# Performance work log

Measured on AMD Instinct MI355X. Metric: run time of the kernel, lower is better.

## Reference

```python
import jax, jax.numpy as jnp
import numpy as np

EPS = 1e-5
NEG = -1e20


def layer_norm(x, gamma, beta):
    mu = jnp.mean(x, axis=-1, keepdims=True)
    var = jnp.mean(jnp.square(x - mu), axis=-1, keepdims=True)
    return (x - mu) * jax.lax.rsqrt(var + EPS) * gamma + beta


def setup_inputs() -> dict:
    key = jax.random.key(0)
    ks = jax.random.split(key, 12)
    B, S, D, H, HD = 2, 2048, 1024, 16, 64
    hid = H * HD
    inp = {
        "q": jax.random.normal(ks[0], (B, S, D), jnp.float32),
        "k": jax.random.normal(ks[1], (B, S, D), jnp.float32),
        "v": jax.random.normal(ks[2], (B, S, D), jnp.float32),
        "mask": jax.random.randint(ks[3], (B, 1, S, S), 0, 2, jnp.int32),
        "Wq": jax.random.normal(ks[4], (D, hid), jnp.float32) * (D ** -0.5),
        "bq": jnp.zeros((hid,), jnp.float32),
        "Wk": jax.random.normal(ks[5], (D, hid), jnp.float32) * (D ** -0.5),
        "bk": jnp.zeros((hid,), jnp.float32),
        "Wv": jax.random.normal(ks[6], (D, hid), jnp.float32) * (D ** -0.5),
        "bv": jnp.zeros((hid,), jnp.float32),
        "Wo": jax.random.normal(ks[7], (hid, D), jnp.float32) * (hid ** -0.5),
        "bo": jnp.zeros((D,), jnp.float32),
        "gamma": jnp.ones((D,), jnp.float32),
        "beta": jnp.zeros((D,), jnp.float32),
    }
    return inp


def reference(q, k, v, mask, Wq, bq, Wk, bk, Wv, bv, Wo, bo, gamma, beta):
    B, S, D = q.shape
    H, HD = 16, 64
    scale = HD ** -0.5
    qh = (layer_norm(q, gamma, beta) @ Wq + bq).reshape(B, S, H, HD).transpose(0, 2, 1, 3)
    kh = (layer_norm(k, gamma, beta) @ Wk + bk).reshape(B, S, H, HD).transpose(0, 2, 1, 3)
    vh = (layer_norm(v, gamma, beta) @ Wv + bv).reshape(B, S, H, HD).transpose(0, 2, 1, 3)
    dots = jnp.einsum('bhqd,bhkd->bhqk', qh, kh)  # [B,H,S,S]
    dots = jnp.where(mask == 0, NEG, dots) * scale  # mask BEFORE scale (as in source)
    attn = jax.nn.softmax(dots, axis=-1)
    out = jnp.einsum('bhqk,bhkd->bhqd', attn, vh)  # [B,H,S,HD]
    # Faithful to `out.view(B, S, -1)` on a [B,H,S,HD]-contiguous tensor: raw reshape,
    # no head transpose.
    out = out.reshape(B, S, H * HD)
    return out @ Wo + bo
```

## Files before the change

### kernel.cpp

```cpp
#include <hip/hip_runtime.h>

typedef short short8 __attribute__((ext_vector_type(8)));
typedef float f32x4 __attribute__((ext_vector_type(4)));

#define QSCALE 0.18033688011112042f

__device__ __forceinline__ unsigned short f2bf(float f) {
  unsigned u = __builtin_bit_cast(unsigned, f);
  u += 0x7fffu + ((u >> 16) & 1u);
  return (unsigned short)(u >> 16);
}

__device__ __forceinline__ void gload16(const void* g, void* l) {
  typedef __attribute__((address_space(1))) unsigned int gas;
  typedef __attribute__((address_space(3))) unsigned int las;
  __builtin_amdgcn_global_load_lds((gas*)(unsigned long long)g,
                                   (las*)(unsigned)(unsigned long long)l, 16, 0, 0);
}

#define MFMA16(a, b, c) __builtin_amdgcn_mfma_f32_16x16x32_bf16(a, b, c, 0, 0, 0)

__global__ __launch_bounds__(256) void wtrans_kernel(
    const float* __restrict__ Wq, const float* __restrict__ Wk,
    const float* __restrict__ Wv, const float* __restrict__ Wo,
    unsigned short* __restrict__ Wt) {
  const int wsel = blockIdx.z;
  const float* W = wsel == 0 ? Wq : wsel == 1 ? Wk : wsel == 2 ? Wv : Wo;
  const float wscale = (wsel == 0) ? QSCALE : 1.0f;
  unsigned short* out = Wt + (long)wsel * 1048576;
  __shared__ float lds[64][65];
  const int t = threadIdx.x;
  const int k0 = blockIdx.x * 64, n0 = blockIdx.y * 64;
#pragma unroll
  for (int i = 0; i < 4; ++i) {
    int r = (t >> 4) + i * 16, c4 = (t & 15) * 4;
    float4 vv = *(const float4*)(W + (long)(k0 + r) * 1024 + n0 + c4);
    lds[r][c4] = vv.x; lds[r][c4 + 1] = vv.y; lds[r][c4 + 2] = vv.z; lds[r][c4 + 3] = vv.w;
  }
  __syncthreads();
#pragma unroll
  for (int i = 0; i < 16; ++i) {
    int flat = t + i * 256;
    int n = flat >> 6, kk = flat & 63;
    out[(long)(n0 + n) * 1024 + k0 + kk] = f2bf(lds[kk][n] * wscale);
  }
}

__global__ __launch_bounds__(256) void maskpack_kernel(const int* __restrict__ mask,
                                                       unsigned* __restrict__ bits) {
  const long n = 8388608;
  const long stride = (long)gridDim.x * 256;
  const int lane = threadIdx.x & 63;
  for (long i = (long)blockIdx.x * 256 + threadIdx.x; i < n; i += stride) {
    unsigned long long bal = __ballot(mask[i] != 0);
    if ((lane & 31) == 0) bits[i >> 5] = (unsigned)(bal >> (lane & 32));
  }
}

__global__ __launch_bounds__(256) void ln_kernel(
    const float* __restrict__ q, const float* __restrict__ k, const float* __restrict__ v,
    const float* __restrict__ gamma, const float* __restrict__ beta,
    unsigned short* __restrict__ lnq, unsigned short* __restrict__ lnk,
    unsigned short* __restrict__ lnv) {
  const int row = blockIdx.x, which = blockIdx.y;
  const float* x = (which == 0 ? q : which == 1 ? k : v) + (long)row * 1024;
  unsigned short* y = (which == 0 ? lnq : which == 1 ? lnk : lnv) + (long)row * 1024;
  const int t = threadIdx.x, lane = t & 63, wv = t >> 6;
  float4 xv = ((const float4*)x)[t];
  float s = xv.x + xv.y + xv.z + xv.w;
  float s2 = xv.x * xv.x + xv.y * xv.y + xv.z * xv.z + xv.w * xv.w;
#pragma unroll
  for (int off = 32; off > 0; off >>= 1) {
    s += __shfl_down(s, off);
    s2 += __shfl_down(s2, off);
  }
  __shared__ float red[8];
  if (lane == 0) { red[wv] = s; red[wv + 4] = s2; }
  __syncthreads();
  float tot = red[0] + red[1] + red[2] + red[3];
  float tot2 = red[4] + red[5] + red[6] + red[7];
  float mu = tot * (1.0f / 1024.0f);
  float var = tot2 * (1.0f / 1024.0f) - mu * mu;
  float rs = rsqrtf(var + 1e-5f);
  float4 g = ((const float4*)gamma)[t];
  float4 be = ((const float4*)beta)[t];
  ushort4 o;
  o.x = f2bf((xv.x - mu) * rs * g.x + be.x);
  o.y = f2bf((xv.y - mu) * rs * g.y + be.y);
  o.z = f2bf((xv.z - mu) * rs * g.z + be.z);
  o.w = f2bf((xv.w - mu) * rs * g.w + be.w);
  ((ushort4*)y)[t] = o;
}

template <int BM, int MODE>
__global__ __launch_bounds__(256) void gemm_kernel(
    const unsigned short* __restrict__ A0, const unsigned short* __restrict__ A1,
    const unsigned short* __restrict__ A2, const unsigned short* __restrict__ Wt,
    const float* __restrict__ b0, const float* __restrict__ b1,
    const float* __restrict__ b2, unsigned short* __restrict__ outB,
    unsigned short* __restrict__ outV, float* __restrict__ outF) {
  constexpr int BK = 64;
  constexpr int MI = BM / 32;
  const int z = blockIdx.z;
  const unsigned short* A = z == 0 ? A0 : z == 1 ? A1 : A2;
  const unsigned short* Bt = Wt + (long)z * 1048576;
  const float* bias = z == 0 ? b0 : z == 1 ? b1 : b2;
  unsigned short* outz = outB + (long)z * 4194304;
  const float bscale = (MODE == 0 && z == 0) ? QSCALE : 1.0f;

  __shared__ char lds[BM * 128 + 16384];
  char* As = lds;
  char* Bs = lds + BM * 128;
  const int tid = threadIdx.x, lane = tid & 63, w = tid >> 6;
  const int wr = w >> 1, wc = w & 1;
  const int m0 = blockIdx.x * BM, n0 = blockIdx.y * 128;
  constexpr int K = 1024;
  constexpr int ACH = BM * 8 / 256;

  f32x4 acc[MI][4] = {};
  for (int kt = 0; kt < K / BK; ++kt) {
    __syncthreads();
#pragma unroll
    for (int i = 0; i < ACH; ++i) {
      int c = tid + i * 256;
      int row = c >> 3, pg = (c & 7) ^ (row & 7);
      gload16(A + (long)(m0 + row) * K + kt * BK + pg * 8, As + c * 16);
    }
#pragma unroll
    for (int i = 0; i < 4; ++i) {
      int c = tid + i * 256;
      int row = c >> 3, pg = (c & 7) ^ (row & 7);
      gload16(Bt + (long)(n0 + row) * K + kt * BK + pg * 8, Bs + c * 16);
    }
    asm volatile("s_waitcnt vmcnt(0)" ::: "memory");
    __syncthreads();
#pragma unroll
    for (int ks = 0; ks < 2; ++ks) {
      short8 af[MI], bf[4];
#pragma unroll
      for (int mi = 0; mi < MI; ++mi) {
        int row = wr * (BM / 2) + mi * 16 + (lane & 15);
        int part = (ks * 4 + (lane >> 4)) ^ (row & 7);
        af[mi] = *(const short8*)(As + row * 128 + part * 16);
      }
#pragma unroll
      for (int ni = 0; ni < 4; ++ni) {
        int row = wc * 64 + ni * 16 + (lane & 15);
        int part = (ks * 4 + (lane >> 4)) ^ (row & 7);
        bf[ni] = *(const short8*)(Bs + row * 128 + part * 16);
      }
#pragma unroll
      for (int mi = 0; mi < MI; ++mi)
#pragma unroll
        for (int ni = 0; ni < 4; ++ni)
          acc[mi][ni] = MFMA16(af[mi], bf[ni], acc[mi][ni]);
    }
  }
#pragma unroll
  for (int mi = 0; mi < MI; ++mi) {
    int mbase = m0 + wr * (BM / 2) + mi * 16 + ((lane >> 4) << 2);
#pragma unroll
    for (int ni = 0; ni < 4; ++ni) {
      int j = n0 + wc * 64 + ni * 16 + (lane & 15);
      float bj = bias[j] * bscale;
      float t0 = acc[mi][ni][0] + bj;
      float t1 = acc[mi][ni][1] + bj;
      float t2 = acc[mi][ni][2] + bj;
      float t3 = acc[mi][ni][3] + bj;
      if constexpr (MODE == 0) {
        int b = mbase >> 11, s = mbase & 2047;
        int h = j >> 6, d = j & 63;
        if (z == 2) {
          unsigned lo, hi;
          asm("v_cvt_pk_bf16_f32 %0, %1, %2" : "=v"(lo) : "v"(t0), "v"(t1));
          asm("v_cvt_pk_bf16_f32 %0, %1, %2" : "=v"(hi) : "v"(t2), "v"(t3));
          uint2 o; o.x = lo; o.y = hi;
          *(uint2*)(outV + ((long)(b * 16 + h) * 64 + d) * 2048 + s) = o;
        } else {
          long base = (((long)(b * 16 + h)) * 2048 + s) * 64 + d;
          outz[base] = f2bf(t0);
          outz[base + 64] = f2bf(t1);
          outz[base + 128] = f2bf(t2);
          outz[base + 192] = f2bf(t3);
        }
      } else {
        outF[(long)mbase * 1024 + j] = t0;
        outF[(long)(mbase + 1) * 1024 + j] = t1;
        outF[(long)(mbase + 2) * 1024 + j] = t2;
        outF[(long)(mbase + 3) * 1024 + j] = t3;
      }
    }
  }
}

__global__ __launch_bounds__(128, 2) void attn_kernel(
    const unsigned short* __restrict__ qh, const unsigned short* __restrict__ kh,
    const unsigned short* __restrict__ vt, const unsigned* __restrict__ mbits,
    unsigned short* __restrict__ O) {
  constexpr int S = 2048, NT = 32;
  __shared__ char lds[40960];
  char* Ks = lds;
  char* Vts = lds + 16384;
  const int tid = threadIdx.x, lane = tid & 63, w = tid >> 6;
  const int g = lane >> 4, c = lane & 15;
  char* Pw = lds + 32768 + w * 4096;

  const int flat = blockIdx.y * 32 + blockIdx.x;
  const int fl2 = (flat & 7) * 128 + (flat >> 3);
  const int qb = fl2 & 31, bh = fl2 >> 5, b = bh >> 4;

  const unsigned short* qp = qh + (long)bh * S * 64;
  const unsigned short* kp = kh + (long)bh * S * 64;
  const unsigned short* vp = vt + (long)bh * 64 * S;
  unsigned short* op = O + (long)bh * S * 64;
  const unsigned* mrow = mbits + (long)b * S * 64;
  const int q0 = qb * 64 + w * 32;
  const int myq0 = q0 + c, myq1 = q0 + 16 + c;

  short8 bq_[2][2];
#pragma unroll
  for (int qg = 0; qg < 2; ++qg)
#pragma unroll
    for (int ds = 0; ds < 2; ++ds)
      bq_[qg][ds] = *(const short8*)(qp + (long)(q0 + qg * 16 + c) * 64 + ds * 32 + g * 8);

  f32x4 o_acc[2][4] = {};
  float lp0 = 0.f, lp1 = 0.f;

#define STAGE(KT, BUF)                                                              \
  {                                                                                 \
    _Pragma("unroll") for (int i = 0; i < 4; ++i) {                                 \
      int cc = tid + i * 128;                                                       \
      int row = cc >> 3, pg = (cc & 7) ^ (row & 7);                                 \
      gload16(kp + (long)((KT)*64 + row) * 64 + pg * 8, Ks + (BUF)*8192 + cc * 16); \
    }                                                                               \
    _Pragma("unroll") for (int i = 0; i < 4; ++i) {                                 \
      int cc = tid + i * 128;                                                       \
      int row = cc >> 3, pg = (cc & 7) ^ (row & 7);                                 \
      gload16(vp + (long)row * S + (KT)*64 + pg * 8, Vts + (BUF)*8192 + cc * 16);   \
    }                                                                               \
  }

#define SOFTMAX(SC, MC, LP, QG)                                                     \
  {                                                                                 \
    unsigned ws0 = MC.x >> (g * 4), ws1 = MC.y >> (g * 4);                          \
    _Pragma("unroll") for (int kf = 0; kf < 4; ++kf) {                              \
      unsigned wsh = ((kf >= 2) ? ws1 : ws0) >> ((kf & 1) * 16);                    \
      float pv0 = __builtin_amdgcn_exp2f(SC[kf][0]);                                \
      float pv1 = __builtin_amdgcn_exp2f(SC[kf][1]);                                \
      float pv2 = __builtin_amdgcn_exp2f(SC[kf][2]);                                \
      float pv3 = __builtin_amdgcn_exp2f(SC[kf][3]);                                \
      pv0 = (wsh & 1u) ? pv0 : 0.f;                                                 \
      pv1 = (wsh & 2u) ? pv1 : 0.f;                                                 \
      pv2 = (wsh & 4u) ? pv2 : 0.f;                                                 \
      pv3 = (wsh & 8u) ? pv3 : 0.f;                                                 \
      LP += (pv0 + pv1) + (pv2 + pv3);                                              \
      unsigned plo, phi;                                                            \
      asm("v_cvt_pk_bf16_f32 %0, %1, %2" : "=v"(plo) : "v"(pv0), "v"(pv1));         \
      asm("v_cvt_pk_bf16_f32 %0, %1, %2" : "=v"(phi) : "v"(pv2), "v"(pv3));         \
      uint2 pk2; pk2.x = plo; pk2.y = phi;                                          \
      int plog = kf * 2 + (g >> 1);                                                 \
      *(uint2*)(Pw + (QG)*2048 + c * 128 + ((plog ^ (c & 7)) * 16) + (g & 1) * 8) = \
          pk2;                                                                      \
    }                                                                               \
  }

#define SUBSTEP(BUF, MC0, MC1)                                                      \
  {                                                                                 \
    f32x4 sc0[4] = {}, sc1[4] = {};                                                 \
    const char* Kb = Ks + (BUF)*8192;                                               \
    __builtin_amdgcn_s_setprio(1);                                                  \
    _Pragma("unroll") for (int ds = 0; ds < 2; ++ds) {                              \
      _Pragma("unroll") for (int kf = 0; kf < 4; ++kf) {                            \
        int row = kf * 16 + c;                                                      \
        int part = (ds * 4 + g) ^ (c & 7);                                          \
        short8 ak = *(const short8*)(Kb + row * 128 + part * 16);                   \
        sc0[kf] = MFMA16(ak, bq_[0][ds], sc0[kf]);                                  \
        sc1[kf] = MFMA16(ak, bq_[1][ds], sc1[kf]);                                  \
      }                                                                             \
    }                                                                               \
    __builtin_amdgcn_s_setprio(0);                                                  \
    SOFTMAX(sc0, MC0, lp0, 0);                                                      \
    SOFTMAX(sc1, MC1, lp1, 1);                                                      \
    const char* Vb = Vts + (BUF)*8192;                                              \
    __builtin_amdgcn_s_setprio(1);                                                  \
    _Pragma("unroll") for (int ks = 0; ks < 2; ++ks) {                              \
      int part = ks * 4 + g;                                                        \
      short8 pa0 = *(const short8*)(Pw + c * 128 + ((part ^ (c & 7)) * 16));        \
      short8 pa1 = *(const short8*)(Pw + 2048 + c * 128 + ((part ^ (c & 7)) * 16)); \
      _Pragma("unroll") for (int nd = 0; nd < 4; ++nd) {                            \
        int d = nd * 16 + c;                                                        \
        short8 bv = *(const short8*)(Vb + d * 128 + ((part ^ (d & 7)) * 16));       \
        o_acc[0][nd] = MFMA16(pa0, bv, o_acc[0][nd]);                               \
        o_acc[1][nd] = MFMA16(pa1, bv, o_acc[1][nd]);                               \
      }                                                                             \
    }                                                                               \
    __builtin_amdgcn_s_setprio(0);                                                  \
    asm volatile("s_waitcnt lgkmcnt(0)" ::: "memory");                              \
    __builtin_amdgcn_s_barrier();                                                   \
  }

  STAGE(0, 0);
  uint2 m0c = *(const uint2*)(mrow + (long)myq0 * 64);
  uint2 m1c = *(const uint2*)(mrow + (long)myq1 * 64);
  uint2 m0n, m1n;

  for (int kt2 = 0; kt2 < NT; kt2 += 2) {
    STAGE(kt2 + 1, 1);
    m0n = *(const uint2*)(mrow + (long)myq0 * 64 + (kt2 + 1) * 2);
    m1n = *(const uint2*)(mrow + (long)myq1 * 64 + (kt2 + 1) * 2);
    asm volatile("s_waitcnt vmcnt(10)" ::: "memory");
    __builtin_amdgcn_s_barrier();
    SUBSTEP(0, m0c, m1c);
    if (kt2 + 2 < NT) {
      STAGE(kt2 + 2, 0);
      m0c = *(const uint2*)(mrow + (long)myq0 * 64 + (kt2 + 2) * 2);
      m1c = *(const uint2*)(mrow + (long)myq1 * 64 + (kt2 + 2) * 2);
      asm volatile("s_waitcnt vmcnt(10)" ::: "memory");
    } else {
      asm volatile("s_waitcnt vmcnt(0)" ::: "memory");
    }
    __builtin_amdgcn_s_barrier();
    SUBSTEP(1, m0n, m1n);
  }
#undef SUBSTEP
#undef SOFTMAX
#undef STAGE

  lp0 += __shfl_xor(lp0, 16);
  lp0 += __shfl_xor(lp0, 32);
  lp1 += __shfl_xor(lp1, 16);
  lp1 += __shfl_xor(lp1, 32);
#pragma unroll
  for (int r = 0; r < 4; ++r) {
    float lr0 = __shfl(lp0, g * 4 + r);
    float lr1 = __shfl(lp1, g * 4 + r);
    float inv0 = 1.0f / lr0;
    float inv1 = 1.0f / lr1;
    int qrow0 = q0 + g * 4 + r;
    int qrow1 = q0 + 16 + g * 4 + r;
#pragma unroll
    for (int nd = 0; nd < 4; ++nd) {
      op[(long)qrow0 * 64 + nd * 16 + c] = f2bf(o_acc[0][nd][r] * inv0);
      op[(long)qrow1 * 64 + nd * 16 + c] = f2bf(o_acc[1][nd][r] * inv1);
    }
  }
}

extern "C" void kernel_launch(void* const* d_in, const int* in_sizes, int n_in,
                              void* d_out, int out_size, void* d_ws, size_t ws_size,
                              hipStream_t stream) {
  const float* q = (const float*)d_in[0];
  const float* k = (const float*)d_in[1];
  const float* v = (const float*)d_in[2];
  const int* mask = (const int*)d_in[3];
  const float* Wq = (const float*)d_in[4];
  const float* bq = (const float*)d_in[5];
  const float* Wk = (const float*)d_in[6];
  const float* bk = (const float*)d_in[7];
  const float* Wv = (const float*)d_in[8];
  const float* bv = (const float*)d_in[9];
  const float* Wo = (const float*)d_in[10];
  const float* bo = (const float*)d_in[11];
  const float* gamma = (const float*)d_in[12];
  const float* beta = (const float*)d_in[13];
  float* out = (float*)d_out;

  char* ws = (char*)d_ws;
  unsigned short* Wt = (unsigned short*)ws;
  unsigned* mbits = (unsigned*)(ws + 8u * 1024 * 1024);
  unsigned short* lnq = (unsigned short*)(ws + 9u * 1024 * 1024);
  unsigned short* lnk = lnq + 4194304;
  unsigned short* lnv = lnk + 4194304;
  unsigned short* qh = lnv + 4194304;
  unsigned short* kh = qh + 4194304;
  unsigned short* vtb = kh + 4194304;
  unsigned short* Ob = lnq;

  wtrans_kernel<<<dim3(16, 16, 4), 256, 0, stream>>>(Wq, Wk, Wv, Wo, Wt);
  maskpack_kernel<<<1024, 256, 0, stream>>>(mask, mbits);
  ln_kernel<<<dim3(4096, 3), 256, 0, stream>>>(q, k, v, gamma, beta, lnq, lnk, lnv);
  gemm_kernel<128, 0><<<dim3(32, 8, 3), 256, 0, stream>>>(lnq, lnk, lnv, Wt, bq, bk, bv,
                                                          qh, vtb, nullptr);
  attn_kernel<<<dim3(32, 32), 128, 0, stream>>>(qh, kh, vtb, mbits, Ob);
  gemm_kernel<128, 1><<<dim3(32, 8, 1), 256, 0, stream>>>(Ob, Ob, Ob, Wt + 3 * 1048576,
                                                          bo, bo, bo, nullptr, nullptr, out);
}
```

Baseline: 160.0 us.

## Switch attention to 32x32x16 MFMA and keep P in registers via permlane swaps

Rewrites the attention inner loop to use 32x32x16 bf16 MFMA tiles instead of 16x16x32, with the score layout computed transposed (K as A operand) so the softmax output can be repacked into the PV MFMA A-operand with v_permlane32_swap rather than round-tripping through LDS. This removes the per-wave P staging buffer in LDS and its write/read traffic, shrinking shared memory. The epilogue and row-sum reductions are adapted to the new lane layout. It relies on a correct permlane mapping and mask bit indexing; register pressure from 16-wide accumulators may change.

```diff
diff --git a/kernel.cpp b/kernel.cpp
--- a/kernel.cpp
+++ b/kernel.cpp
@@ -2,6 +2,7 @@
 
 typedef short short8 __attribute__((ext_vector_type(8)));
 typedef float f32x4 __attribute__((ext_vector_type(4)));
+typedef float f32x16 __attribute__((ext_vector_type(16)));
 
 #define QSCALE 0.18033688011112042f
 
@@ -18,7 +19,14 @@
                                    (las*)(unsigned)(unsigned long long)l, 16, 0, 0);
 }
 
+__device__ __forceinline__ short8 mk8(unsigned r0, unsigned r1, unsigned r2, unsigned r3) {
+  union { unsigned u[4]; short8 s; } t;
+  t.u[0] = r0; t.u[1] = r1; t.u[2] = r2; t.u[3] = r3;
+  return t.s;
+}
+
 #define MFMA16(a, b, c) __builtin_amdgcn_mfma_f32_16x16x32_bf16(a, b, c, 0, 0, 0)
+#define MFMA32(a, b, c) __builtin_amdgcn_mfma_f32_32x32x16_bf16(a, b, c, 0, 0, 0)
 
 __global__ __launch_bounds__(256) void wtrans_kernel(
     const float* __restrict__ Wq, const float* __restrict__ Wk,
@@ -198,12 +206,11 @@
     const unsigned short* __restrict__ vt, const unsigned* __restrict__ mbits,
     unsigned short* __restrict__ O) {
   constexpr int S = 2048, NT = 32;
-  __shared__ char lds[40960];
+  __shared__ char lds[32768];
   char* Ks = lds;
   char* Vts = lds + 16384;
   const int tid = threadIdx.x, lane = tid & 63, w = tid >> 6;
-  const int g = lane >> 4, c = lane & 15;
-  char* Pw = lds + 32768 + w * 4096;
+  const int qc = lane & 31, h = lane >> 5;
 
   const int flat = blockIdx.y * 32 + blockIdx.x;
   const int fl2 = (flat & 7) * 128 + (flat >> 3);
@@ -215,17 +222,15 @@
   unsigned short* op = O + (long)bh * S * 64;
   const unsigned* mrow = mbits + (long)b * S * 64;
   const int q0 = qb * 64 + w * 32;
-  const int myq0 = q0 + c, myq1 = q0 + 16 + c;
-
-  short8 bq_[2][2];
-#pragma unroll
-  for (int qg = 0; qg < 2; ++qg)
-#pragma unroll
-    for (int ds = 0; ds < 2; ++ds)
-      bq_[qg][ds] = *(const short8*)(qp + (long)(q0 + qg * 16 + c) * 64 + ds * 32 + g * 8);
-
-  f32x4 o_acc[2][4] = {};
-  float lp0 = 0.f, lp1 = 0.f;
+  const int myq = q0 + qc;
+
+  short8 bq_[4];
+#pragma unroll
+  for (int ds4 = 0; ds4 < 4; ++ds4)
+    bq_[ds4] = *(const short8*)(qp + (long)myq * 64 + ds4 * 16 + h * 8);
+
+  f32x16 o_acc[2] = {};
+  float lp = 0.f;
 
 #define STAGE(KT, BUF)                                                              \
   {                                                                                 \
@@ -241,59 +246,61 @@
     }                                                                               \
   }
 
-#define SOFTMAX(SC, MC, LP, QG)                                                     \
+#define SM32(SC, MW, PA0, PA1)                                                      \
   {                                                                                 \
-    unsigned ws0 = MC.x >> (g * 4), ws1 = MC.y >> (g * 4);                          \
-    _Pragma("unroll") for (int kf = 0; kf < 4; ++kf) {                              \
-      unsigned wsh = ((kf >= 2) ? ws1 : ws0) >> ((kf & 1) * 16);                    \
-      float pv0 = __builtin_amdgcn_exp2f(SC[kf][0]);                                \
-      float pv1 = __builtin_amdgcn_exp2f(SC[kf][1]);                                \
-      float pv2 = __builtin_amdgcn_exp2f(SC[kf][2]);                                \
-      float pv3 = __builtin_amdgcn_exp2f(SC[kf][3]);                                \
-      pv0 = (wsh & 1u) ? pv0 : 0.f;                                                 \
-      pv1 = (wsh & 2u) ? pv1 : 0.f;                                                 \
-      pv2 = (wsh & 4u) ? pv2 : 0.f;                                                 \
-      pv3 = (wsh & 8u) ? pv3 : 0.f;                                                 \
-      LP += (pv0 + pv1) + (pv2 + pv3);                                              \
-      unsigned plo, phi;                                                            \
-      asm("v_cvt_pk_bf16_f32 %0, %1, %2" : "=v"(plo) : "v"(pv0), "v"(pv1));         \
-      asm("v_cvt_pk_bf16_f32 %0, %1, %2" : "=v"(phi) : "v"(pv2), "v"(pv3));         \
-      uint2 pk2; pk2.x = plo; pk2.y = phi;                                          \
-      int plog = kf * 2 + (g >> 1);                                                 \
-      *(uint2*)(Pw + (QG)*2048 + c * 128 + ((plog ^ (c & 7)) * 16) + (g & 1) * 8) = \
-          pk2;                                                                      \
-    }                                                                               \
-  }
-
-#define SUBSTEP(BUF, MC0, MC1)                                                      \
+    unsigned wsh = (MW) >> (h * 4);                                                 \
+    float p[16];                                                                    \
+    _Pragma("unroll") for (int r = 0; r < 16; ++r) {                                \
+      float e = __builtin_amdgcn_exp2f(SC[r]);                                      \
+      int bit = (r & 3) + 8 * (r >> 2);                                             \
+      p[r] = ((wsh >> bit) & 1u) ? e : 0.f;                                         \
+      lp += p[r];                                                                   \
+    }                                                                               \
+    unsigned a0, b0, c0, d0, a1, b1, c1, d1;                                        \
+    asm("v_cvt_pk_bf16_f32 %0, %1, %2" : "=v"(a0) : "v"(p[0]), "v"(p[1]));          \
+    asm("v_cvt_pk_bf16_f32 %0, %1, %2" : "=v"(c0) : "v"(p[2]), "v"(p[3]));          \
+    asm("v_cvt_pk_bf16_f32 %0, %1, %2" : "=v"(b0) : "v"(p[4]), "v"(p[5]));          \
+    asm("v_cvt_pk_bf16_f32 %0, %1, %2" : "=v"(d0) : "v"(p[6]), "v"(p[7]));          \
+    asm("v_cvt_pk_bf16_f32 %0, %1, %2" : "=v"(a1) : "v"(p[8]), "v"(p[9]));          \
+    asm("v_cvt_pk_bf16_f32 %0, %1, %2" : "=v"(c1) : "v"(p[10]), "v"(p[11]));        \
+    asm("v_cvt_pk_bf16_f32 %0, %1, %2" : "=v"(b1) : "v"(p[12]), "v"(p[13]));        \
+    asm("v_cvt_pk_bf16_f32 %0, %1, %2" : "=v"(d1) : "v"(p[14]), "v"(p[15]));        \
+    asm("v_permlane32_swap_b32 %0, %1" : "+v"(a0), "+v"(b0));                       \
+    asm("v_permlane32_swap_b32 %0, %1" : "+v"(c0), "+v"(d0));                       \
+    asm("v_permlane32_swap_b32 %0, %1" : "+v"(a1), "+v"(b1));                       \
+    asm("v_permlane32_swap_b32 %0, %1" : "+v"(c1), "+v"(d1));                       \
+    PA0 = mk8(a0, c0, b0, d0);                                                      \
+    PA1 = mk8(a1, c1, b1, d1);                                                      \
+  }
+
+#define SUBSTEP(BUF, MC)                                                            \
   {                                                                                 \
-    f32x4 sc0[4] = {}, sc1[4] = {};                                                 \
+    f32x16 sc0 = {}, sc1 = {};                                                      \
     const char* Kb = Ks + (BUF)*8192;                                               \
     __builtin_amdgcn_s_setprio(1);                                                  \
-    _Pragma("unroll") for (int ds = 0; ds < 2; ++ds) {                              \
-      _Pragma("unroll") for (int kf = 0; kf < 4; ++kf) {                            \
-        int row = kf * 16 + c;                                                      \
-        int part = (ds * 4 + g) ^ (c & 7);                                          \
-        short8 ak = *(const short8*)(Kb + row * 128 + part * 16);                   \
-        sc0[kf] = MFMA16(ak, bq_[0][ds], sc0[kf]);                                  \
-        sc1[kf] = MFMA16(ak, bq_[1][ds], sc1[kf]);                                  \
-      }                                                                             \
+    _Pragma("unroll") for (int ds4 = 0; ds4 < 4; ++ds4) {                           \
+      int part = (ds4 * 2 + h) ^ (qc & 7);                                          \
+      short8 ak0 = *(const short8*)(Kb + qc * 128 + part * 16);                     \
+      short8 ak1 = *(const short8*)(Kb + (32 + qc) * 128 + part * 16);              \
+      sc0 = MFMA32(ak0, bq_[ds4], sc0);                                             \
+      sc1 = MFMA32(ak1, bq_[ds4], sc1);                                             \
     }                                                                               \
     __builtin_amdgcn_s_setprio(0);                                                  \
-    SOFTMAX(sc0, MC0, lp0, 0);                                                      \
-    SOFTMAX(sc1, MC1, lp1, 1);                                                      \
+    short8 pa00, pa01, pa10, pa11;                                                  \
+    SM32(sc0, MC.x, pa00, pa01);                                                    \
+    SM32(sc1, MC.y, pa10, pa11);                                                    \
     const char* Vb = Vts + (BUF)*8192;                                              \
     __builtin_amdgcn_s_setprio(1);                                                  \
-    _Pragma("unroll") for (int ks = 0; ks < 2; ++ks) {                              \
-      int part = ks * 4 + g;                                                        \
-      short8 pa0 = *(const short8*)(Pw + c * 128 + ((part ^ (c & 7)) * 16));        \
-      short8 pa1 = *(const short8*)(Pw + 2048 + c * 128 + ((part ^ (c & 7)) * 16)); \
-      _Pragma("unroll") for (int nd = 0; nd < 4; ++nd) {                            \
-        int d = nd * 16 + c;                                                        \
-        short8 bv = *(const short8*)(Vb + d * 128 + ((part ^ (d & 7)) * 16));       \
-        o_acc[0][nd] = MFMA16(pa0, bv, o_acc[0][nd]);                               \
-        o_acc[1][nd] = MFMA16(pa1, bv, o_acc[1][nd]);                               \
-      }                                                                             \
+    _Pragma("unroll") for (int nd = 0; nd < 2; ++nd) {                              \
+      const char* vr = Vb + (nd * 32 + qc) * 128;                                   \
+      short8 bv0 = *(const short8*)(vr + ((0 + h) ^ (qc & 7)) * 16);                \
+      o_acc[nd] = MFMA32(pa00, bv0, o_acc[nd]);                                     \
+      short8 bv1 = *(const short8*)(vr + ((2 + h) ^ (qc & 7)) * 16);                \
+      o_acc[nd] = MFMA32(pa01, bv1, o_acc[nd]);                                     \
+      short8 bv2 = *(const short8*)(vr + ((4 + h) ^ (qc & 7)) * 16);                \
+      o_acc[nd] = MFMA32(pa10, bv2, o_acc[nd]);                                     \
+      short8 bv3 = *(const short8*)(vr + ((6 + h) ^ (qc & 7)) * 16);                \
+      o_acc[nd] = MFMA32(pa11, bv3, o_acc[nd]);                                     \
     }                                                                               \
     __builtin_amdgcn_s_setprio(0);                                                  \
     asm volatile("s_waitcnt lgkmcnt(0)" ::: "memory");                              \
@@ -301,49 +308,37 @@
   }
 
   STAGE(0, 0);
-  uint2 m0c = *(const uint2*)(mrow + (long)myq0 * 64);
-  uint2 m1c = *(const uint2*)(mrow + (long)myq1 * 64);
-  uint2 m0n, m1n;
+  uint2 mcur = *(const uint2*)(mrow + (long)myq * 64);
+  uint2 mnxt = mcur;
 
   for (int kt2 = 0; kt2 < NT; kt2 += 2) {
     STAGE(kt2 + 1, 1);
-    m0n = *(const uint2*)(mrow + (long)myq0 * 64 + (kt2 + 1) * 2);
-    m1n = *(const uint2*)(mrow + (long)myq1 * 64 + (kt2 + 1) * 2);
-    asm volatile("s_waitcnt vmcnt(10)" ::: "memory");
+    mnxt = *(const uint2*)(mrow + (long)myq * 64 + (kt2 + 1) * 2);
+    asm volatile("s_waitcnt vmcnt(9)" ::: "memory");
     __builtin_amdgcn_s_barrier();
-    SUBSTEP(0, m0c, m1c);
+    SUBSTEP(0, mcur);
     if (kt2 + 2 < NT) {
       STAGE(kt2 + 2, 0);
-      m0c = *(const uint2*)(mrow + (long)myq0 * 64 + (kt2 + 2) * 2);
-      m1c = *(const uint2*)(mrow + (long)myq1 * 64 + (kt2 + 2) * 2);
-      asm volatile("s_waitcnt vmcnt(10)" ::: "memory");
+      mcur = *(const uint2*)(mrow + (long)myq * 64 + (kt2 + 2) * 2);
+      asm volatile("s_waitcnt vmcnt(9)" ::: "memory");
     } else {
       asm volatile("s_waitcnt vmcnt(0)" ::: "memory");
     }
     __builtin_amdgcn_s_barrier();
-    SUBSTEP(1, m0n, m1n);
+    SUBSTEP(1, mnxt);
   }
 #undef SUBSTEP
-#undef SOFTMAX
+#undef SM32
 #undef STAGE
 
-  lp0 += __shfl_xor(lp0, 16);
-  lp0 += __shfl_xor(lp0, 32);
-  lp1 += __shfl_xor(lp1, 16);
-  lp1 += __shfl_xor(lp1, 32);
-#pragma unroll
-  for (int r = 0; r < 4; ++r) {
-    float lr0 = __shfl(lp0, g * 4 + r);
-    float lr1 = __shfl(lp1, g * 4 + r);
-    float inv0 = 1.0f / lr0;
-    float inv1 = 1.0f / lr1;
-    int qrow0 = q0 + g * 4 + r;
-    int qrow1 = q0 + 16 + g * 4 + r;
-#pragma unroll
-    for (int nd = 0; nd < 4; ++nd) {
-      op[(long)qrow0 * 64 + nd * 16 + c] = f2bf(o_acc[0][nd][r] * inv0);
-      op[(long)qrow1 * 64 + nd * 16 + c] = f2bf(o_acc[1][nd][r] * inv1);
-    }
+  lp += __shfl_xor(lp, 32);
+#pragma unroll
+  for (int r = 0; r < 16; ++r) {
+    int ql = (r & 3) + 8 * (r >> 2) + 4 * h;
+    float inv = 1.0f / __shfl(lp, ql);
+    long qrow = q0 + ql;
+    op[qrow * 64 + qc] = f2bf(o_acc[0][r] * inv);
+    op[qrow * 64 + 32 + qc] = f2bf(o_acc[1][r] * inv);
   }
 }
 
```

New measurement: 168.4 us. 1.05x slower.
